# Kernel tuning notes

Hardware: AMD Instinct MI355X
Metric: run time of the kernel (lower is better)

The kernel has to match this reference:

```python
import jax, jax.numpy as jnp
import numpy as np
from jax import lax

DIM = 96; DSTATE = 16; DCONV = 3; EXPAND = 2
DINNER = DIM * EXPAND            # 192
DTRANK = (DIM + 15) // 16        # 6 = ceil(dim/16)
B = 4; H = 48; W = 48
BN_EPS = 1e-3
LN_EPS = 1e-5


def setup_inputs() -> dict:
    key = jax.random.key(0)
    ks = iter(jax.random.split(key, 32))
    def n(shape, s):
        return jax.random.normal(next(ks), shape, dtype=jnp.float32) * s
    inp = {}
    inp["feature"] = jax.random.normal(next(ks), (B, DIM, H, W), dtype=jnp.float32)
    inp["prediction"] = jax.random.normal(next(ks), (B, 1, H, W), dtype=jnp.float32)
    # norm_pred: BatchNorm2d(1) (eval mode, running stats)
    inp["bnp_g"] = jnp.ones((1,), jnp.float32)
    inp["bnp_b"] = jnp.zeros((1,), jnp.float32)
    inp["bnp_m"] = n((1,), 0.1)
    inp["bnp_v"] = jnp.ones((1,), jnp.float32) + jax.random.uniform(next(ks), (1,)) * 0.1
    # pre_proj: Conv1x1(no bias) + BN + GELU
    inp["pre_w"] = n((DIM, DIM), 0.05)
    inp["pre_bn_g"] = jnp.ones((DIM,), jnp.float32)
    inp["pre_bn_b"] = jnp.zeros((DIM,), jnp.float32)
    inp["pre_bn_m"] = n((DIM,), 0.1)
    inp["pre_bn_v"] = jnp.ones((DIM,), jnp.float32) + jax.random.uniform(next(ks), (DIM,)) * 0.1
    # norm_feature: LayerNorm(dim)
    inp["ln_g"] = jnp.ones((DIM,), jnp.float32)
    inp["ln_b"] = jnp.zeros((DIM,), jnp.float32)
    # SS2D params (VMamba)
    inp["in_proj_w"] = n((2 * DINNER, DIM), 0.05)
    inp["conv_w"] = n((DINNER, 1, DCONV, DCONV), 0.1)   # depthwise
    inp["conv_b"] = jnp.zeros((DINNER,), jnp.float32)
    inp["x_proj_w"] = n((4, DTRANK + 2 * DSTATE, DINNER), 0.05)
    inp["dt_w"] = n((4, DINNER, DTRANK), 0.1)
    inp["dt_b"] = n((4, DINNER), 0.1)
    # S4D-real init: A = -exp(A_logs), A_logs = log(1..N)
    inp["A_logs"] = jnp.log(jnp.tile(jnp.arange(1, DSTATE + 1, dtype=jnp.float32), (4 * DINNER, 1)))
    inp["Ds"] = jnp.ones((4 * DINNER,), jnp.float32)
    inp["onorm_g"] = jnp.ones((DINNER,), jnp.float32)
    inp["onorm_b"] = jnp.zeros((DINNER,), jnp.float32)
    inp["out_proj_w"] = n((DIM, DINNER), 0.05)
    # post_proj: Conv1x1(no bias) + BN + GELU
    inp["post_w"] = n((DIM, DIM), 0.05)
    inp["post_bn_g"] = jnp.ones((DIM,), jnp.float32)
    inp["post_bn_b"] = jnp.zeros((DIM,), jnp.float32)
    inp["post_bn_m"] = n((DIM,), 0.1)
    inp["post_bn_v"] = jnp.ones((DIM,), jnp.float32) + jax.random.uniform(next(ks), (DIM,)) * 0.1
    inp["gate"] = jnp.ones((1,), jnp.float32) * 0.5
    return inp


def _bn(x, g, b, m, v):
    # x: [B,C,H,W]; per-channel eval-mode batchnorm, eps=1e-3
    scale = g / jnp.sqrt(v + BN_EPS)
    return (x - m[None, :, None, None]) * scale[None, :, None, None] + b[None, :, None, None]


def _ln(x, g, b):
    mu = jnp.mean(x, axis=-1, keepdims=True)
    var = jnp.var(x, axis=-1, keepdims=True)
    return (x - mu) / jnp.sqrt(var + LN_EPS) * g + b


def _selective_scan(xs, dts, As, Bs, Cs, Ds, dt_bias):
    # xs,dts: [B,4,D,L]; As: [4,D,N]; Bs,Cs: [B,4,N,L]; Ds,dt_bias: [4,D]
    delta = jax.nn.softplus(dts + dt_bias[None, :, :, None])   # [B,4,D,L]
    u_t = jnp.moveaxis(xs, -1, 0)      # [L,B,4,D]
    d_t = jnp.moveaxis(delta, -1, 0)   # [L,B,4,D]
    B_t = jnp.moveaxis(Bs, -1, 0)      # [L,B,4,N]
    C_t = jnp.moveaxis(Cs, -1, 0)      # [L,B,4,N]
    h0 = jnp.zeros(xs.shape[:3] + (As.shape[-1],), xs.dtype)   # [B,4,D,N]
    def step(h, inp):
        u, d, Bm, Cm = inp
        dA = jnp.exp(d[..., None] * As[None])                     # [B,4,D,N]
        h = h * dA + (d * u)[..., None] * Bm[:, :, None, :]
        y = jnp.einsum('bkdn,bkn->bkd', h, Cm)
        return h, y
    _, ys = lax.scan(step, h0, (u_t, d_t, B_t, C_t))
    y = jnp.moveaxis(ys, 0, -1)        # [B,4,D,L]
    return y + Ds[None, :, :, None] * xs


def _ss2d(x_cl, in_proj_w, conv_w, conv_b, x_proj_w, dt_w, dt_b, A_logs, Ds,
          onorm_g, onorm_b, out_proj_w):
    Bsz, Hh, Ww, _ = x_cl.shape
    di = conv_w.shape[0]
    L = Hh * Ww
    xz = jnp.einsum('bhwc,oc->bhwo', x_cl, in_proj_w)
    x, z = jnp.split(xz, 2, axis=-1)
    xc = jnp.transpose(x, (0, 3, 1, 2))                           # [B,di,H,W]
    pad = (DCONV - 1) // 2
    xc = lax.conv_general_dilated(xc, conv_w, (1, 1), [(pad, pad), (pad, pad)],
                                  dimension_numbers=('NCHW', 'OIHW', 'NCHW'),
                                  feature_group_count=di) + conv_b[None, :, None, None]
    xc = jax.nn.silu(xc)
    # cross-scan: row-major, col-major, and their reverses
    x0 = xc.reshape(Bsz, di, L)
    x1 = jnp.transpose(xc, (0, 1, 3, 2)).reshape(Bsz, di, L)
    xhw = jnp.stack([x0, x1], axis=1)                             # [B,2,di,L]
    xs = jnp.concatenate([xhw, jnp.flip(xhw, axis=-1)], axis=1)   # [B,4,di,L]
    x_dbl = jnp.einsum('bkdl,kcd->bkcl', xs, x_proj_w)
    dts = x_dbl[:, :, :DTRANK]
    Bs = x_dbl[:, :, DTRANK:DTRANK + DSTATE]
    Cs = x_dbl[:, :, DTRANK + DSTATE:]
    dts = jnp.einsum('bkrl,kdr->bkdl', dts, dt_w)
    As = -jnp.exp(A_logs).reshape(4, di, DSTATE)
    out_y = _selective_scan(xs, dts, As, Bs, Cs, Ds.reshape(4, di), dt_b)  # [B,4,di,L]
    inv_y = jnp.flip(out_y[:, 2:4], axis=-1)
    wh = jnp.transpose(out_y[:, 1].reshape(Bsz, di, Ww, Hh), (0, 1, 3, 2)).reshape(Bsz, di, L)
    invwh = jnp.transpose(inv_y[:, 1].reshape(Bsz, di, Ww, Hh), (0, 1, 3, 2)).reshape(Bsz, di, L)
    y = out_y[:, 0] + inv_y[:, 0] + wh + invwh                    # [B,di,L]
    y = jnp.transpose(y.reshape(Bsz, di, Hh, Ww), (0, 2, 3, 1))   # [B,H,W,di]
    y = _ln(y, onorm_g, onorm_b)
    y = y * jax.nn.silu(z)
    return jnp.einsum('bhwd,od->bhwo', y, out_proj_w)


def reference(feature, prediction, bnp_g, bnp_b, bnp_m, bnp_v,
              pre_w, pre_bn_g, pre_bn_b, pre_bn_m, pre_bn_v, ln_g, ln_b,
              in_proj_w, conv_w, conv_b, x_proj_w, dt_w, dt_b, A_logs, Ds,
              onorm_g, onorm_b, out_proj_w,
              post_w, post_bn_g, post_bn_b, post_bn_m, post_bn_v, gate):
    pred_norm = _bn(prediction, bnp_g, bnp_b, bnp_m, bnp_v)
    reverse_mask = 1.0 - jax.nn.sigmoid(pred_norm)
    fm = feature * reverse_mask
    fp = jax.nn.gelu(_bn(jnp.einsum('bchw,oc->bohw', fm, pre_w),
                         pre_bn_g, pre_bn_b, pre_bn_m, pre_bn_v), approximate=False)
    x_cl = _ln(jnp.transpose(fp, (0, 2, 3, 1)), ln_g, ln_b)
    y = _ss2d(x_cl, in_proj_w, conv_w, conv_b, x_proj_w, dt_w, dt_b, A_logs, Ds,
              onorm_g, onorm_b, out_proj_w)
    yr = jnp.transpose(y, (0, 3, 1, 2))
    yr = jax.nn.gelu(_bn(jnp.einsum('bchw,oc->bohw', yr, post_w),
                         post_bn_g, post_bn_b, post_bn_m, post_bn_v), approximate=False)
    return feature + gate[0] * yr
```

## Files before the change

kernel.cpp:

```cpp
#include <hip/hip_runtime.h>
#include <math.h>

#define RFL(x) __builtin_amdgcn_readfirstlane(x)

constexpr int CDIM = 96;
constexpr int DI   = 192;
constexpr int HW   = 48;
constexpr int LL   = 2304;
constexpr int NK   = 4;
constexpr int DST  = 16;
constexpr int DTRK = 6;
constexpr int NCH  = 48;
constexpr int CHK  = 48;
constexpr float LOG2E  = 1.44269504088896f;
constexpr float CBN_EPS = 1e-3f;
constexpr float CLN_EPS = 1e-5f;

__device__ __forceinline__ int Tmap(int x){ return (x % HW) * HW + x / HW; }
__device__ __forceinline__ float siluf(float x){ return x / (1.f + __expf(-x)); }
__device__ __forceinline__ float geluf(float x){ return 0.5f * x * (1.f + erff(x * 0.70710678118654752f)); }
__device__ __forceinline__ int permp(int k, int l){
  if (k == 0) return l;
  if (k == 1) return Tmap(l);
  if (k == 2) return LL - 1 - l;
  return Tmap(LL - 1 - l);
}
__device__ __forceinline__ int lmap(int k, int p){
  if (k == 0) return p;
  if (k == 1) return Tmap(p);
  if (k == 2) return LL - 1 - p;
  return LL - 1 - Tmap(p);
}

__global__ __launch_bounds__(256) void mrr_k0_wcomb(
    const float* __restrict__ post_w, const float* __restrict__ opw, float* __restrict__ Wc)
{
  int idx = blockIdx.x * 256 + threadIdx.x;
  int o = idx / DI, d = idx % DI;
  float acc = 0.f;
  for (int c = 0; c < CDIM; ++c)
    acc = fmaf(post_w[o * CDIM + c], opw[c * DI + d], acc);
  Wc[idx] = acc;
}

__global__ __launch_bounds__(256) void mrr_k1_pre(
    const float* __restrict__ feature, const float* __restrict__ pred,
    const float* __restrict__ bnp_g, const float* __restrict__ bnp_b,
    const float* __restrict__ bnp_m, const float* __restrict__ bnp_v,
    const float* __restrict__ pre_w,
    const float* __restrict__ pbg, const float* __restrict__ pbb,
    const float* __restrict__ pbm, const float* __restrict__ pbv,
    const float* __restrict__ lng, const float* __restrict__ lnb,
    float* __restrict__ x_cl)
{
  __shared__ float s_fm[CDIM][64];
  __shared__ float s_red[8][64];
  __shared__ float s_mu[64], s_rs[64];
  int tid = threadIdx.x;
  int b = blockIdx.x / 36, p0 = (blockIdx.x % 36) * 64;

  if (tid < 64) {
    float pr = pred[b * LL + p0 + tid];
    float sc = bnp_g[0] * rsqrtf(bnp_v[0] + CBN_EPS);
    float pn = (pr - bnp_m[0]) * sc + bnp_b[0];
    s_mu[tid] = 1.f - 1.f / (1.f + __expf(-pn));
  }
  __syncthreads();
  #pragma unroll
  for (int e = 0; e < 24; ++e) {
    int f = e * 256 + tid;
    int c = f >> 6, px = f & 63;
    s_fm[c][px] = feature[(size_t)(b * CDIM + c) * LL + p0 + px] * s_mu[px];
  }
  __syncthreads();
  int lane = tid & 63;
  int wave = tid >> 6;
  int oc0 = RFL(wave * 24);
  float acc[24];
  #pragma unroll
  for (int j = 0; j < 24; ++j) acc[j] = 0.f;
  for (int c = 0; c < CDIM; c += 4) {
    float f0 = s_fm[c][lane], f1 = s_fm[c+1][lane];
    float f2 = s_fm[c+2][lane], f3 = s_fm[c+3][lane];
    #pragma unroll
    for (int j = 0; j < 24; ++j) {
      float4 w = *(const float4*)&pre_w[(oc0 + j) * CDIM + c];
      acc[j] = fmaf(w.x, f0, fmaf(w.y, f1, fmaf(w.z, f2, fmaf(w.w, f3, acc[j]))));
    }
  }
  float s = 0.f, s2 = 0.f;
  #pragma unroll
  for (int j = 0; j < 24; ++j) {
    int oc = oc0 + j;
    float sc = pbg[oc] * rsqrtf(pbv[oc] + CBN_EPS);
    float v = (acc[j] - pbm[oc]) * sc + pbb[oc];
    v = geluf(v);
    acc[j] = v; s += v; s2 = fmaf(v, v, s2);
  }
  s_red[wave][lane] = s; s_red[4 + wave][lane] = s2;
  __syncthreads();
  if (tid < 64) {
    float t1 = s_red[0][tid] + s_red[1][tid] + s_red[2][tid] + s_red[3][tid];
    float t2 = s_red[4][tid] + s_red[5][tid] + s_red[6][tid] + s_red[7][tid];
    float mu = t1 * (1.f / 96.f);
    float var = t2 * (1.f / 96.f) - mu * mu;
    s_mu[tid] = mu; s_rs[tid] = rsqrtf(var + CLN_EPS);
  }
  __syncthreads();
  float mu = s_mu[lane], rs = s_rs[lane];
  #pragma unroll
  for (int j = 0; j < 24; ++j) {
    int oc = oc0 + j;
    acc[j] = (acc[j] - mu) * rs * lng[oc] + lnb[oc];
  }
  float* dst = &x_cl[(size_t)(b * LL + p0 + lane) * CDIM + oc0];
  #pragma unroll
  for (int j = 0; j < 24; j += 4)
    *(float4*)(dst + j) = make_float4(acc[j], acc[j+1], acc[j+2], acc[j+3]);
}

__global__ __launch_bounds__(1024) void mrr_k2_inproj(
    const float* __restrict__ x_cl, const float* __restrict__ ipw,
    float* __restrict__ xb, float* __restrict__ szb)
{
  __shared__ float s_x[CDIM][65];
  int tid = threadIdx.x;
  int b = blockIdx.x / 36, p0 = (blockIdx.x % 36) * 64;
  #pragma unroll
  for (int e = 0; e < 6; ++e) {
    int f = e * 1024 + tid;
    int c = f % CDIM, px = f / CDIM;
    s_x[c][px] = x_cl[(size_t)(b * LL + p0 + px) * CDIM + c];
  }
  __syncthreads();
  int lane = tid & 63;
  int oc0 = RFL((tid >> 6) * 24);
  float acc[24];
  #pragma unroll
  for (int j = 0; j < 24; ++j) acc[j] = 0.f;
  for (int c = 0; c < CDIM; c += 4) {
    float f0 = s_x[c][lane], f1 = s_x[c+1][lane];
    float f2 = s_x[c+2][lane], f3 = s_x[c+3][lane];
    #pragma unroll
    for (int j = 0; j < 24; ++j) {
      float4 w = *(const float4*)&ipw[(oc0 + j) * CDIM + c];
      acc[j] = fmaf(w.x, f0, fmaf(w.y, f1, fmaf(w.z, f2, fmaf(w.w, f3, acc[j]))));
    }
  }
  int p = p0 + lane;
  if (oc0 < DI) {
    float* dst = &xb[(size_t)(b * LL + p) * DI + oc0];
    #pragma unroll
    for (int j = 0; j < 24; j += 4)
      *(float4*)(dst + j) = make_float4(acc[j], acc[j+1], acc[j+2], acc[j+3]);
  } else {
    #pragma unroll
    for (int j = 0; j < 24; ++j) acc[j] = siluf(acc[j]);
    float* dst = &szb[(size_t)(b * LL + p) * DI + (oc0 - DI)];
    #pragma unroll
    for (int j = 0; j < 24; j += 4)
      *(float4*)(dst + j) = make_float4(acc[j], acc[j+1], acc[j+2], acc[j+3]);
  }
}

__global__ __launch_bounds__(256) void mrr_k3_conv(
    const float* __restrict__ xb, const float* __restrict__ cw,
    const float* __restrict__ cb, float* __restrict__ xc)
{
  int idx = blockIdx.x * 256 + threadIdx.x;
  int d = idx % DI;
  int p = (idx / DI) % LL;
  int b = idx / (DI * LL);
  int h = p / HW, w = p % HW;
  float acc = cb[d];
  #pragma unroll
  for (int i = 0; i < 3; ++i) {
    int hh = h + i - 1;
    if (hh < 0 || hh >= HW) continue;
    #pragma unroll
    for (int j = 0; j < 3; ++j) {
      int ww = w + j - 1;
      if (ww < 0 || ww >= HW) continue;
      acc = fmaf(cw[d * 9 + i * 3 + j], xb[(size_t)(b * LL + hh * HW + ww) * DI + d], acc);
    }
  }
  xc[idx] = siluf(acc);
}

__global__ __launch_bounds__(640) void mrr_k4_proj(
    const float* __restrict__ xc, const float* __restrict__ xpw,
    const float* __restrict__ dtw, const float* __restrict__ dtb,
    float* __restrict__ delta, float* __restrict__ Bsb, float* __restrict__ Csb)
{
  __shared__ float s_u[DI][72];
  __shared__ float s_w[48][164];
  __shared__ float s_dtr[NK][DTRK][64];
  __shared__ float s_dtwf[NK * DI * DTRK];
  __shared__ float s_dtbf[NK * DI];
  int tid = threadIdx.x;
  int b = blockIdx.x / 36, p0 = (blockIdx.x % 36) * 64;
  int b4 = b * NK;

  for (int f = tid; f < DI * 64; f += 640) {
    int d_ = f % DI, px = f / DI;
    s_u[d_][px] = xc[(size_t)(b * LL + p0 + px) * DI + d_];
  }
  for (int f = tid; f < NK * DI * DTRK; f += 640) s_dtwf[f] = dtw[f];
  for (int f = tid; f < NK * DI; f += 640) s_dtbf[f] = dtb[f];

  int rg = tid >> 4;
  int pg = tid & 15;
  float acc[4][4];
  #pragma unroll
  for (int i = 0; i < 4; ++i)
    #pragma unroll
    for (int j = 0; j < 4; ++j) acc[i][j] = 0.f;

  for (int ch = 0; ch < 4; ++ch) {
    int c0 = ch * 48;
    if (ch) __syncthreads();
    for (int f = tid; f < 152 * 48; f += 640) {
      int cl = f % 48, row = f / 48;
      int kk = row / 38, rr = row % 38;
      s_w[cl][kk * 40 + rr] = xpw[row * DI + c0 + cl];
    }
    __syncthreads();
    #pragma unroll 4
    for (int cc = 0; cc < 48; ++cc) {
      float4 wv = *(const float4*)&s_w[cc][rg << 2];
      float4 uv = *(const float4*)&s_u[c0 + cc][pg << 2];
      acc[0][0] = fmaf(wv.x, uv.x, acc[0][0]); acc[0][1] = fmaf(wv.x, uv.y, acc[0][1]);
      acc[0][2] = fmaf(wv.x, uv.z, acc[0][2]); acc[0][3] = fmaf(wv.x, uv.w, acc[0][3]);
      acc[1][0] = fmaf(wv.y, uv.x, acc[1][0]); acc[1][1] = fmaf(wv.y, uv.y, acc[1][1]);
      acc[1][2] = fmaf(wv.y, uv.z, acc[1][2]); acc[1][3] = fmaf(wv.y, uv.w, acc[1][3]);
      acc[2][0] = fmaf(wv.z, uv.x, acc[2][0]); acc[2][1] = fmaf(wv.z, uv.y, acc[2][1]);
      acc[2][2] = fmaf(wv.z, uv.z, acc[2][2]); acc[2][3] = fmaf(wv.z, uv.w, acc[2][3]);
      acc[3][0] = fmaf(wv.w, uv.x, acc[3][0]); acc[3][1] = fmaf(wv.w, uv.y, acc[3][1]);
      acc[3][2] = fmaf(wv.w, uv.z, acc[3][2]); acc[3][3] = fmaf(wv.w, uv.w, acc[3][3]);
    }
  }

  #pragma unroll
  for (int i = 0; i < 4; ++i) {
    int rp = (rg << 2) + i;
    int kk = rp / 40, rr = rp % 40;
    if (rr < DTRK) {
      #pragma unroll
      for (int j = 0; j < 4; ++j) s_dtr[kk][rr][(pg << 2) + j] = acc[i][j];
    } else if (rr < DTRK + DST) {
      int n = rr - DTRK;
      #pragma unroll
      for (int j = 0; j < 4; ++j) {
        int l = lmap(kk, p0 + (pg << 2) + j);
        Bsb[(size_t)((b4 + kk) * LL + l) * DST + n] = acc[i][j];
      }
    } else if (rr < DTRK + 2 * DST) {
      int n = rr - DTRK - DST;
      #pragma unroll
      for (int j = 0; j < 4; ++j) {
        int l = lmap(kk, p0 + (pg << 2) + j);
        Csb[(size_t)((b4 + kk) * LL + l) * DST + n] = acc[i][j];
      }
    }
  }
  __syncthreads();

  int lane = tid & 63;
  int wv_ = tid >> 6;
  for (int unit = wv_; unit < 64; unit += 10) {
    int kk = unit >> 4, pxq = unit & 15;
    float dtr[6][4];
    #pragma unroll
    for (int rr = 0; rr < 6; ++rr)
      #pragma unroll
      for (int j = 0; j < 4; ++j)
        dtr[rr][j] = s_dtr[kk][rr][(pxq << 2) + j];
    #pragma unroll
    for (int dch = 0; dch < 3; ++dch) {
      int d_ = dch * 64 + lane;
      int kdl = kk * DI + d_;
      float w0 = s_dtwf[kdl * 6 + 0], w1 = s_dtwf[kdl * 6 + 1], w2 = s_dtwf[kdl * 6 + 2];
      float w3 = s_dtwf[kdl * 6 + 3], w4 = s_dtwf[kdl * 6 + 4], w5 = s_dtwf[kdl * 6 + 5];
      float bias = s_dtbf[kdl];
      #pragma unroll
      for (int j = 0; j < 4; ++j) {
        float sv = bias;
        sv = fmaf(w0, dtr[0][j], sv); sv = fmaf(w1, dtr[1][j], sv);
        sv = fmaf(w2, dtr[2][j], sv); sv = fmaf(w3, dtr[3][j], sv);
        sv = fmaf(w4, dtr[4][j], sv); sv = fmaf(w5, dtr[5][j], sv);
        float sp = fmaxf(sv, 0.f) + __logf(1.f + __expf(-fabsf(sv)));
        int l = lmap(kk, p0 + (pxq << 2) + j);
        delta[(size_t)((b4 + kk) * LL + l) * DI + d_] = sp;
      }
    }
  }
}

#define SSTEP(n, Bc, Cc) { float dA = exp2f(A2[n] * dv); hh[n] = fmaf(hh[n], dA, du * (Bc)); y = fmaf(hh[n], (Cc), y); }

__global__ __launch_bounds__(256) void mrr_k5_scan1(
    const float* __restrict__ delta, const float* __restrict__ xc,
    const float* __restrict__ Bsb, const float* __restrict__ Csb,
    const float* __restrict__ A_logs,
    float* __restrict__ yb, float* __restrict__ hend, float* __restrict__ Ssum)
{
  int lane = threadIdx.x & 63;
  int wid = RFL(blockIdx.x * 4 + (threadIdx.x >> 6));
  int c = wid % NCH;
  int r = wid / NCH;
  int dch = r % 3;
  int k = (r / 3) % NK;
  int b = r / (3 * NK);
  int d = dch * 64 + lane;
  int kd = k * DI + d;

  float A2[16];
  {
    const float4* Ap = (const float4*)&A_logs[(size_t)kd * 16];
    #pragma unroll
    for (int i = 0; i < 4; ++i) {
      float4 a = Ap[i];
      A2[4*i+0] = -exp2f(a.x * LOG2E) * LOG2E;
      A2[4*i+1] = -exp2f(a.y * LOG2E) * LOG2E;
      A2[4*i+2] = -exp2f(a.z * LOG2E) * LOG2E;
      A2[4*i+3] = -exp2f(a.w * LOG2E) * LOG2E;
    }
  }
  float hh[16];
  #pragma unroll
  for (int n = 0; n < 16; ++n) hh[n] = 0.f;
  float S = 0.f;
  int l0 = c * CHK;
  int bk = b * NK + k;
  size_t ebase = (size_t)(bk * LL + l0) * DI + d;
  size_t bbase = (size_t)(bk * LL + l0) * DST;
  float dv = delta[ebase];
  float u  = xc[(size_t)(b * LL + permp(k, l0)) * DI + d];
  const float4* Bp = (const float4*)(Bsb + bbase);
  const float4* Cp = (const float4*)(Csb + bbase);
  float4 B0 = Bp[0], B1 = Bp[1], B2 = Bp[2], B3 = Bp[3];
  float4 C0 = Cp[0], C1 = Cp[1], C2 = Cp[2], C3 = Cp[3];
  for (int t = 0; t < CHK; ++t) {
    int tn = (t < CHK - 1) ? t + 1 : t;
    float ndv = delta[ebase + (size_t)tn * DI];
    float nu  = xc[(size_t)(b * LL + permp(k, l0 + tn)) * DI + d];
    const float4* nBp = (const float4*)(Bsb + bbase + (size_t)tn * DST);
    const float4* nCp = (const float4*)(Csb + bbase + (size_t)tn * DST);
    float4 nB0 = nBp[0], nB1 = nBp[1], nB2 = nBp[2], nB3 = nBp[3];
    float4 nC0 = nCp[0], nC1 = nCp[1], nC2 = nCp[2], nC3 = nCp[3];
    float du = dv * u;
    float y = 0.f;
    SSTEP(0,  B0.x, C0.x) SSTEP(1,  B0.y, C0.y) SSTEP(2,  B0.z, C0.z) SSTEP(3,  B0.w, C0.w)
    SSTEP(4,  B1.x, C1.x) SSTEP(5,  B1.y, C1.y) SSTEP(6,  B1.z, C1.z) SSTEP(7,  B1.w, C1.w)
    SSTEP(8,  B2.x, C2.x) SSTEP(9,  B2.y, C2.y) SSTEP(10, B2.z, C2.z) SSTEP(11, B2.w, C2.w)
    SSTEP(12, B3.x, C3.x) SSTEP(13, B3.y, C3.y) SSTEP(14, B3.z, C3.z) SSTEP(15, B3.w, C3.w)
    yb[ebase + (size_t)t * DI] = y;
    S += dv;
    dv = ndv; u = nu;
    B0 = nB0; B1 = nB1; B2 = nB2; B3 = nB3;
    C0 = nC0; C1 = nC1; C2 = nC2; C3 = nC3;
  }
  int gg = bk * 3 + dch;
  size_t hb = ((size_t)(gg * NCH + c) * 64 + lane) * 16;
  float4* Hp = (float4*)&hend[hb];
  Hp[0] = make_float4(hh[0], hh[1], hh[2], hh[3]);
  Hp[1] = make_float4(hh[4], hh[5], hh[6], hh[7]);
  Hp[2] = make_float4(hh[8], hh[9], hh[10], hh[11]);
  Hp[3] = make_float4(hh[12], hh[13], hh[14], hh[15]);
  Ssum[(size_t)(gg * NCH + c) * 64 + lane] = S;
}

__global__ __launch_bounds__(1024) void mrr_k5_mid(
    const float* __restrict__ hend, const float* __restrict__ Ssum,
    const float* __restrict__ A_logs, float* __restrict__ hinit)
{
  int t = blockIdx.x * 1024 + threadIdx.x;
  int n = t & 15;
  int g = t >> 4;
  int ln = g & 63;
  int gg = g >> 6;
  int dch = gg % 3;
  int k = (gg / 3) % NK;
  int d = dch * 64 + ln;
  float AL = A_logs[(size_t)(k * DI + d) * 16 + n];
  float A2 = -exp2f(AL * LOG2E) * LOG2E;
  float hi = 0.f;
  for (int c = 0; c < NCH; ++c) {
    size_t a = ((size_t)(gg * NCH + c) * 64 + ln) * 16 + n;
    hinit[a] = hi;
    float S = Ssum[(size_t)(gg * NCH + c) * 64 + ln];
    hi = hend[a] + exp2f(A2 * S) * hi;
  }
}

#define CSTEP(n, Cc) { float e = exp2f(A2[n] * cum); corr = fmaf(e * gi[n], (Cc), corr); }

__global__ __launch_bounds__(256) void mrr_k5_scan2(
    const float* __restrict__ delta, const float* __restrict__ Csb,
    const float* __restrict__ A_logs, const float* __restrict__ hinit,
    float* __restrict__ yb)
{
  int lane = threadIdx.x & 63;
  int wid = RFL(blockIdx.x * 4 + (threadIdx.x >> 6));
  int c = wid % NCH;
  if (c == 0) return;
  int r = wid / NCH;
  int dch = r % 3;
  int k = (r / 3) % NK;
  int b = r / (3 * NK);
  int d = dch * 64 + lane;
  int kd = k * DI + d;
  float A2[16];
  {
    const float4* Ap = (const float4*)&A_logs[(size_t)kd * 16];
    #pragma unroll
    for (int i = 0; i < 4; ++i) {
      float4 a = Ap[i];
      A2[4*i+0] = -exp2f(a.x * LOG2E) * LOG2E;
      A2[4*i+1] = -exp2f(a.y * LOG2E) * LOG2E;
      A2[4*i+2] = -exp2f(a.z * LOG2E) * LOG2E;
      A2[4*i+3] = -exp2f(a.w * LOG2E) * LOG2E;
    }
  }
  int bk = b * NK + k;
  int gg = bk * 3 + dch;
  float gi[16];
  {
    const float4* Gp = (const float4*)&hinit[((size_t)(gg * NCH + c) * 64 + lane) * 16];
    float4 g0 = Gp[0], g1 = Gp[1], g2 = Gp[2], g3 = Gp[3];
    gi[0]=g0.x; gi[1]=g0.y; gi[2]=g0.z; gi[3]=g0.w;
    gi[4]=g1.x; gi[5]=g1.y; gi[6]=g1.z; gi[7]=g1.w;
    gi[8]=g2.x; gi[9]=g2.y; gi[10]=g2.z; gi[11]=g2.w;
    gi[12]=g3.x; gi[13]=g3.y; gi[14]=g3.z; gi[15]=g3.w;
  }
  int l0 = c * CHK;
  size_t ebase = (size_t)(bk * LL + l0) * DI + d;
  size_t bbase = (size_t)(bk * LL + l0) * DST;
  float cum = 0.f;
  float dv = delta[ebase];
  const float4* Cp = (const float4*)(Csb + bbase);
  float4 C0 = Cp[0], C1 = Cp[1], C2 = Cp[2], C3 = Cp[3];
  for (int t = 0; t < CHK; ++t) {
    int tn = (t < CHK - 1) ? t + 1 : t;
    float ndv = delta[ebase + (size_t)tn * DI];
    const float4* nCp = (const float4*)(Csb + bbase + (size_t)tn * DST);
    float4 nC0 = nCp[0], nC1 = nCp[1], nC2 = nCp[2], nC3 = nCp[3];
    cum += dv;
    float corr = 0.f;
    CSTEP(0,  C0.x) CSTEP(1,  C0.y) CSTEP(2,  C0.z) CSTEP(3,  C0.w)
    CSTEP(4,  C1.x) CSTEP(5,  C1.y) CSTEP(6,  C1.z) CSTEP(7,  C1.w)
    CSTEP(8,  C2.x) CSTEP(9,  C2.y) CSTEP(10, C2.z) CSTEP(11, C2.w)
    CSTEP(12, C3.x) CSTEP(13, C3.y) CSTEP(14, C3.z) CSTEP(15, C3.w)
    yb[ebase + (size_t)t * DI] += corr;
    dv = ndv;
    C0 = nC0; C1 = nC1; C2 = nC2; C3 = nC3;
  }
}

__global__ __launch_bounds__(1024) void mrr_k6_out(
    const float* __restrict__ yb, const float* __restrict__ xc,
    const float* __restrict__ szb, const float* __restrict__ Ds,
    const float* __restrict__ ong, const float* __restrict__ onb,
    const float* __restrict__ Wc,
    const float* __restrict__ qbg, const float* __restrict__ qbb,
    const float* __restrict__ qbm, const float* __restrict__ qbv,
    const float* __restrict__ feature, const float* __restrict__ gate,
    float* __restrict__ out)
{
  __shared__ float s_t[DI][65];
  __shared__ float s_red[32][64];
  __shared__ float s_mu[64], s_rs[64];
  int tid = threadIdx.x;
  int b = blockIdx.x / 36, p0 = (blockIdx.x % 36) * 64;
  int b4 = b * NK;
  #pragma unroll
  for (int e = 0; e < 12; ++e) {
    int f = e * 1024 + tid;
    int d = f % DI, px = f / DI;
    int p = p0 + px;
    int tp = Tmap(p);
    float t0 = yb[(size_t)((b4 + 0) * LL + p) * DI + d];
    float t1 = yb[(size_t)((b4 + 1) * LL + tp) * DI + d];
    float t2 = yb[(size_t)((b4 + 2) * LL + (LL - 1 - p)) * DI + d];
    float t3 = yb[(size_t)((b4 + 3) * LL + (LL - 1 - tp)) * DI + d];
    float Dv = Ds[d] + Ds[DI + d] + Ds[2 * DI + d] + Ds[3 * DI + d];
    float tv = t0 + t1 + t2 + t3 + Dv * xc[(size_t)(b * LL + p) * DI + d];
    s_t[d][px] = tv;
  }
  __syncthreads();
  {
    int q = tid >> 6, px = tid & 63;
    float s = 0.f, s2 = 0.f;
    #pragma unroll
    for (int i = 0; i < 12; ++i) {
      float v = s_t[q * 12 + i][px];
      s += v; s2 = fmaf(v, v, s2);
    }
    s_red[q][px] = s; s_red[16 + q][px] = s2;
  }
  __syncthreads();
  if (tid < 64) {
    float s = 0.f, s2 = 0.f;
    #pragma unroll
    for (int q = 0; q < 16; ++q) { s += s_red[q][tid]; s2 += s_red[16 + q][tid]; }
    float mu = s * (1.f / (float)DI);
    float var = s2 * (1.f / (float)DI) - mu * mu;
    s_mu[tid] = mu; s_rs[tid] = rsqrtf(var + CLN_EPS);
  }
  __syncthreads();
  #pragma unroll
  for (int e = 0; e < 12; ++e) {
    int f = e * 1024 + tid;
    int d = f % DI, px = f / DI;
    int p = p0 + px;
    float v = s_t[d][px];
    v = (v - s_mu[px]) * s_rs[px] * ong[d] + onb[d];
    v *= szb[(size_t)(b * LL + p) * DI + d];
    s_t[d][px] = v;
  }
  __syncthreads();
  int lane = tid & 63;
  int o0 = RFL((tid >> 6) * 6);
  float acc[6] = {0.f, 0.f, 0.f, 0.f, 0.f, 0.f};
  for (int dd = 0; dd < DI; dd += 4) {
    float f0 = s_t[dd][lane], f1 = s_t[dd+1][lane];
    float f2 = s_t[dd+2][lane], f3 = s_t[dd+3][lane];
    #pragma unroll
    for (int j = 0; j < 6; ++j) {
      float4 w = *(const float4*)&Wc[(o0 + j) * DI + dd];
      acc[j] = fmaf(w.x, f0, fmaf(w.y, f1, fmaf(w.z, f2, fmaf(w.w, f3, acc[j]))));
    }
  }
  float gt = gate[0];
  #pragma unroll
  for (int j = 0; j < 6; ++j) {
    int o = o0 + j;
    float sc = qbg[o] * rsqrtf(qbv[o] + CBN_EPS);
    float v = (acc[j] - qbm[o]) * sc + qbb[o];
    v = geluf(v);
    size_t oi = (size_t)(b * CDIM + o) * LL + p0 + lane;
    out[oi] = feature[oi] + gt * v;
  }
}

extern "C" void kernel_launch(void* const* d_in, const int* in_sizes, int n_in,
                              void* d_out, int out_size, void* d_ws, size_t ws_size,
                              hipStream_t stream)
{
  (void)in_sizes; (void)n_in; (void)out_size; (void)ws_size;
  const float* feature    = (const float*)d_in[0];
  const float* prediction = (const float*)d_in[1];
  const float* bnp_g      = (const float*)d_in[2];
  const float* bnp_b      = (const float*)d_in[3];
  const float* bnp_m      = (const float*)d_in[4];
  const float* bnp_v      = (const float*)d_in[5];
  const float* pre_w      = (const float*)d_in[6];
  const float* pre_bn_g   = (const float*)d_in[7];
  const float* pre_bn_b   = (const float*)d_in[8];
  const float* pre_bn_m   = (const float*)d_in[9];
  const float* pre_bn_v   = (const float*)d_in[10];
  const float* ln_g       = (const float*)d_in[11];
  const float* ln_b       = (const float*)d_in[12];
  const float* in_proj_w  = (const float*)d_in[13];
  const float* conv_w     = (const float*)d_in[14];
  const float* conv_b     = (const float*)d_in[15];
  const float* x_proj_w   = (const float*)d_in[16];
  const float* dt_w       = (const float*)d_in[17];
  const float* dt_b       = (const float*)d_in[18];
  const float* A_logs     = (const float*)d_in[19];
  const float* Ds         = (const float*)d_in[20];
  const float* onorm_g    = (const float*)d_in[21];
  const float* onorm_b    = (const float*)d_in[22];
  const float* out_proj_w = (const float*)d_in[23];
  const float* post_w     = (const float*)d_in[24];
  const float* post_bn_g  = (const float*)d_in[25];
  const float* post_bn_b  = (const float*)d_in[26];
  const float* post_bn_m  = (const float*)d_in[27];
  const float* post_bn_v  = (const float*)d_in[28];
  const float* gate       = (const float*)d_in[29];
  float* out = (float*)d_out;

  float* ws    = (float*)d_ws;
  float* Wc    = ws;
  float* x_cl  = Wc    + 18432;
  float* xb    = x_cl  + 884736;
  float* szb   = xb    + 1769472;
  float* xcb   = szb   + 1769472;
  float* dlt   = xcb   + 1769472;
  float* Bsb   = dlt   + 7077888;
  float* Csb   = Bsb   + 589824;
  float* yb    = Csb   + 589824;
  float* hend  = yb    + 7077888;
  float* hinit = hend  + 2359296;
  float* Ss    = hinit + 2359296;

  mrr_k0_wcomb<<<dim3(72), dim3(256), 0, stream>>>(post_w, out_proj_w, Wc);
  mrr_k1_pre<<<dim3(144), dim3(256), 0, stream>>>(feature, prediction,
      bnp_g, bnp_b, bnp_m, bnp_v, pre_w,
      pre_bn_g, pre_bn_b, pre_bn_m, pre_bn_v, ln_g, ln_b, x_cl);
  mrr_k2_inproj<<<dim3(144), dim3(1024), 0, stream>>>(x_cl, in_proj_w, xb, szb);
  mrr_k3_conv<<<dim3(6912), dim3(256), 0, stream>>>(xb, conv_w, conv_b, xcb);
  mrr_k4_proj<<<dim3(144), dim3(640), 0, stream>>>(xcb, x_proj_w, dt_w, dt_b, dlt, Bsb, Csb);
  mrr_k5_scan1<<<dim3(576), dim3(256), 0, stream>>>(dlt, xcb, Bsb, Csb, A_logs, yb, hend, Ss);
  mrr_k5_mid<<<dim3(48), dim3(1024), 0, stream>>>(hend, Ss, A_logs, hinit);
  mrr_k5_scan2<<<dim3(576), dim3(256), 0, stream>>>(dlt, Csb, A_logs, hinit, yb);
  mrr_k6_out<<<dim3(144), dim3(1024), 0, stream>>>(yb, xcb, szb, Ds, onorm_g, onorm_b,
      Wc, post_bn_g, post_bn_b, post_bn_m, post_bn_v, feature, gate, out);
}
```

Measured before the change: 388.5 us.

## Split kernels into more blocks, vectorise conv, store cumulative delta for scan2

Several kernels are repartitioned into smaller blocks (pre, inproj, out) so the GPU runs more workgroups. The depthwise conv now handles four channels per thread with float4 loads, using a transposed weight buffer. The scan uses twice as many chunks of half the length and splits the y accumulation across four independent registers. scan1 writes the running delta sum over delta in place, so scan2 reads it directly instead of re-accumulating. The middle pass converts hend to hinit in place, and together with the larger chunk count this changes the workspace layout and adds more inter-chunk serial work.

```diff
diff --git a/kernel.cpp b/kernel.cpp
--- a/kernel.cpp
+++ b/kernel.cpp
@@ -10,8 +10,8 @@
 constexpr int NK   = 4;
 constexpr int DST  = 16;
 constexpr int DTRK = 6;
-constexpr int NCH  = 48;
-constexpr int CHK  = 48;
+constexpr int NCH  = 96;
+constexpr int CHK  = 24;
 constexpr float LOG2E  = 1.44269504088896f;
 constexpr float CBN_EPS = 1e-3f;
 constexpr float CLN_EPS = 1e-5f;
@@ -33,14 +33,21 @@
 }
 
 __global__ __launch_bounds__(256) void mrr_k0_wcomb(
-    const float* __restrict__ post_w, const float* __restrict__ opw, float* __restrict__ Wc)
+    const float* __restrict__ post_w, const float* __restrict__ opw,
+    const float* __restrict__ conv_w, float* __restrict__ Wc, float* __restrict__ cwT)
 {
   int idx = blockIdx.x * 256 + threadIdx.x;
-  int o = idx / DI, d = idx % DI;
-  float acc = 0.f;
-  for (int c = 0; c < CDIM; ++c)
-    acc = fmaf(post_w[o * CDIM + c], opw[c * DI + d], acc);
-  Wc[idx] = acc;
+  if (idx < CDIM * DI) {
+    int o = idx / DI, d = idx % DI;
+    float acc = 0.f;
+    for (int c = 0; c < CDIM; ++c)
+      acc = fmaf(post_w[o * CDIM + c], opw[c * DI + d], acc);
+    Wc[idx] = acc;
+  } else if (idx < CDIM * DI + 9 * DI) {
+    int t = idx - CDIM * DI;
+    int tap = t / DI, d = t % DI;
+    cwT[tap * DI + d] = conv_w[d * 9 + tap];
+  }
 }
 
 __global__ __launch_bounds__(256) void mrr_k1_pre(
@@ -53,88 +60,95 @@
     const float* __restrict__ lng, const float* __restrict__ lnb,
     float* __restrict__ x_cl)
 {
-  __shared__ float s_fm[CDIM][64];
-  __shared__ float s_red[8][64];
-  __shared__ float s_mu[64], s_rs[64];
+  __shared__ float s_fm[CDIM][33];
+  __shared__ float s_red[16][32];
+  __shared__ float s_mu[32], s_rs[32], s_msk[32];
   int tid = threadIdx.x;
-  int b = blockIdx.x / 36, p0 = (blockIdx.x % 36) * 64;
-
-  if (tid < 64) {
+  int b = blockIdx.x / 72, p0 = (blockIdx.x % 72) * 32;
+
+  if (tid < 32) {
     float pr = pred[b * LL + p0 + tid];
     float sc = bnp_g[0] * rsqrtf(bnp_v[0] + CBN_EPS);
     float pn = (pr - bnp_m[0]) * sc + bnp_b[0];
-    s_mu[tid] = 1.f - 1.f / (1.f + __expf(-pn));
-  }
-  __syncthreads();
-  #pragma unroll
-  for (int e = 0; e < 24; ++e) {
+    s_msk[tid] = 1.f - 1.f / (1.f + __expf(-pn));
+  }
+  __syncthreads();
+  #pragma unroll
+  for (int e = 0; e < 12; ++e) {
     int f = e * 256 + tid;
-    int c = f >> 6, px = f & 63;
-    s_fm[c][px] = feature[(size_t)(b * CDIM + c) * LL + p0 + px] * s_mu[px];
+    int c = f >> 5, px = f & 31;
+    s_fm[c][px] = feature[(size_t)(b * CDIM + c) * LL + p0 + px] * s_msk[px];
   }
   __syncthreads();
   int lane = tid & 63;
   int wave = tid >> 6;
-  int oc0 = RFL(wave * 24);
-  float acc[24];
-  #pragma unroll
-  for (int j = 0; j < 24; ++j) acc[j] = 0.f;
+  int px = lane & 31, oh = lane >> 5;
+  int o0 = wave * 24 + oh * 12;
+  float acc[12];
+  #pragma unroll
+  for (int j = 0; j < 12; ++j) acc[j] = 0.f;
   for (int c = 0; c < CDIM; c += 4) {
-    float f0 = s_fm[c][lane], f1 = s_fm[c+1][lane];
-    float f2 = s_fm[c+2][lane], f3 = s_fm[c+3][lane];
-    #pragma unroll
-    for (int j = 0; j < 24; ++j) {
-      float4 w = *(const float4*)&pre_w[(oc0 + j) * CDIM + c];
+    float f0 = s_fm[c][px], f1 = s_fm[c+1][px];
+    float f2 = s_fm[c+2][px], f3 = s_fm[c+3][px];
+    #pragma unroll
+    for (int j = 0; j < 12; ++j) {
+      float4 w = *(const float4*)&pre_w[(o0 + j) * CDIM + c];
       acc[j] = fmaf(w.x, f0, fmaf(w.y, f1, fmaf(w.z, f2, fmaf(w.w, f3, acc[j]))));
     }
   }
   float s = 0.f, s2 = 0.f;
   #pragma unroll
-  for (int j = 0; j < 24; ++j) {
-    int oc = oc0 + j;
+  for (int j = 0; j < 12; ++j) {
+    int oc = o0 + j;
     float sc = pbg[oc] * rsqrtf(pbv[oc] + CBN_EPS);
     float v = (acc[j] - pbm[oc]) * sc + pbb[oc];
     v = geluf(v);
     acc[j] = v; s += v; s2 = fmaf(v, v, s2);
   }
-  s_red[wave][lane] = s; s_red[4 + wave][lane] = s2;
-  __syncthreads();
-  if (tid < 64) {
-    float t1 = s_red[0][tid] + s_red[1][tid] + s_red[2][tid] + s_red[3][tid];
-    float t2 = s_red[4][tid] + s_red[5][tid] + s_red[6][tid] + s_red[7][tid];
+  int grp = wave * 2 + oh;
+  s_red[grp][px] = s; s_red[8 + grp][px] = s2;
+  __syncthreads();
+  if (tid < 32) {
+    float t1 = 0.f, t2 = 0.f;
+    #pragma unroll
+    for (int q = 0; q < 8; ++q) { t1 += s_red[q][tid]; t2 += s_red[8 + q][tid]; }
     float mu = t1 * (1.f / 96.f);
     float var = t2 * (1.f / 96.f) - mu * mu;
     s_mu[tid] = mu; s_rs[tid] = rsqrtf(var + CLN_EPS);
   }
   __syncthreads();
-  float mu = s_mu[lane], rs = s_rs[lane];
-  #pragma unroll
-  for (int j = 0; j < 24; ++j) {
-    int oc = oc0 + j;
+  float mu = s_mu[px], rs = s_rs[px];
+  #pragma unroll
+  for (int j = 0; j < 12; ++j) {
+    int oc = o0 + j;
     acc[j] = (acc[j] - mu) * rs * lng[oc] + lnb[oc];
   }
-  float* dst = &x_cl[(size_t)(b * LL + p0 + lane) * CDIM + oc0];
-  #pragma unroll
-  for (int j = 0; j < 24; j += 4)
+  float* dst = &x_cl[(size_t)(b * LL + p0 + px) * CDIM + o0];
+  #pragma unroll
+  for (int j = 0; j < 12; j += 4)
     *(float4*)(dst + j) = make_float4(acc[j], acc[j+1], acc[j+2], acc[j+3]);
 }
 
-__global__ __launch_bounds__(1024) void mrr_k2_inproj(
+__global__ __launch_bounds__(256) void mrr_k2_inproj(
     const float* __restrict__ x_cl, const float* __restrict__ ipw,
     float* __restrict__ xb, float* __restrict__ szb)
 {
   __shared__ float s_x[CDIM][65];
   int tid = threadIdx.x;
-  int b = blockIdx.x / 36, p0 = (blockIdx.x % 36) * 64;
-  #pragma unroll
-  for (int e = 0; e < 6; ++e) {
-    int f = e * 1024 + tid;
+  int blk = blockIdx.x;
+  int b = blk / 144;
+  int rem = blk % 144;
+  int p0 = (rem % 36) * 64;
+  int q = rem / 36;
+  #pragma unroll
+  for (int e = 0; e < 24; ++e) {
+    int f = e * 256 + tid;
     int c = f % CDIM, px = f / CDIM;
     s_x[c][px] = x_cl[(size_t)(b * LL + p0 + px) * CDIM + c];
   }
   __syncthreads();
   int lane = tid & 63;
-  int oc0 = RFL((tid >> 6) * 24);
+  int oc0 = RFL(q * 96 + (tid >> 6) * 24);
   float acc[24];
   #pragma unroll
   for (int j = 0; j < 24; ++j) acc[j] = 0.f;
@@ -164,15 +178,15 @@
 }
 
 __global__ __launch_bounds__(256) void mrr_k3_conv(
-    const float* __restrict__ xb, const float* __restrict__ cw,
+    const float* __restrict__ xb, const float* __restrict__ cwT,
     const float* __restrict__ cb, float* __restrict__ xc)
 {
   int idx = blockIdx.x * 256 + threadIdx.x;
-  int d = idx % DI;
-  int p = (idx / DI) % LL;
-  int b = idx / (DI * LL);
+  int dg = idx % 48;
+  int p = (idx / 48) % LL;
+  int b = idx / (48 * LL);
   int h = p / HW, w = p % HW;
-  float acc = cb[d];
+  float4 acc = ((const float4*)cb)[dg];
   #pragma unroll
   for (int i = 0; i < 3; ++i) {
     int hh = h + i - 1;
@@ -181,10 +195,16 @@
     for (int j = 0; j < 3; ++j) {
       int ww = w + j - 1;
       if (ww < 0 || ww >= HW) continue;
-      acc = fmaf(cw[d * 9 + i * 3 + j], xb[(size_t)(b * LL + hh * HW + ww) * DI + d], acc);
-    }
-  }
-  xc[idx] = siluf(acc);
+      float4 wv = ((const float4*)&cwT[(i * 3 + j) * DI])[dg];
+      float4 xv = *(const float4*)&xb[(size_t)(b * LL + hh * HW + ww) * DI + dg * 4];
+      acc.x = fmaf(wv.x, xv.x, acc.x);
+      acc.y = fmaf(wv.y, xv.y, acc.y);
+      acc.z = fmaf(wv.z, xv.z, acc.z);
+      acc.w = fmaf(wv.w, xv.w, acc.w);
+    }
+  }
+  acc.x = siluf(acc.x); acc.y = siluf(acc.y); acc.z = siluf(acc.z); acc.w = siluf(acc.w);
+  *(float4*)&xc[(size_t)(b * LL + p) * DI + dg * 4] = acc;
 }
 
 __global__ __launch_bounds__(640) void mrr_k4_proj(
@@ -296,12 +316,13 @@
   }
 }
 
-#define SSTEP(n, Bc, Cc) { float dA = exp2f(A2[n] * dv); hh[n] = fmaf(hh[n], dA, du * (Bc)); y = fmaf(hh[n], (Cc), y); }
+#define SSTEP(n, Bc, Cc, yy) { float dA = exp2f(A2[n] * dv); hh[n] = fmaf(hh[n], dA, du * (Bc)); yy = fmaf(hh[n], (Cc), yy); }
 
 __global__ __launch_bounds__(256) void mrr_k5_scan1(
-    const float* __restrict__ delta, const float* __restrict__ xc,
+    const float* __restrict__ xc,
     const float* __restrict__ Bsb, const float* __restrict__ Csb,
     const float* __restrict__ A_logs,
+    float* __restrict__ delta,
     float* __restrict__ yb, float* __restrict__ hend, float* __restrict__ Ssum)
 {
   int lane = threadIdx.x & 63;
@@ -349,13 +370,14 @@
     float4 nB0 = nBp[0], nB1 = nBp[1], nB2 = nBp[2], nB3 = nBp[3];
     float4 nC0 = nCp[0], nC1 = nCp[1], nC2 = nCp[2], nC3 = nCp[3];
     float du = dv * u;
-    float y = 0.f;
-    SSTEP(0,  B0.x, C0.x) SSTEP(1,  B0.y, C0.y) SSTEP(2,  B0.z, C0.z) SSTEP(3,  B0.w, C0.w)
-    SSTEP(4,  B1.x, C1.x) SSTEP(5,  B1.y, C1.y) SSTEP(6,  B1.z, C1.z) SSTEP(7,  B1.w, C1.w)
-    SSTEP(8,  B2.x, C2.x) SSTEP(9,  B2.y, C2.y) SSTEP(10, B2.z, C2.z) SSTEP(11, B2.w, C2.w)
-    SSTEP(12, B3.x, C3.x) SSTEP(13, B3.y, C3.y) SSTEP(14, B3.z, C3.z) SSTEP(15, B3.w, C3.w)
-    yb[ebase + (size_t)t * DI] = y;
+    float y0 = 0.f, y1 = 0.f, y2 = 0.f, y3 = 0.f;
+    SSTEP(0,  B0.x, C0.x, y0) SSTEP(1,  B0.y, C0.y, y1) SSTEP(2,  B0.z, C0.z, y2) SSTEP(3,  B0.w, C0.w, y3)
+    SSTEP(4,  B1.x, C1.x, y0) SSTEP(5,  B1.y, C1.y, y1) SSTEP(6,  B1.z, C1.z, y2) SSTEP(7,  B1.w, C1.w, y3)
+    SSTEP(8,  B2.x, C2.x, y0) SSTEP(9,  B2.y, C2.y, y1) SSTEP(10, B2.z, C2.z, y2) SSTEP(11, B2.w, C2.w, y3)
+    SSTEP(12, B3.x, C3.x, y0) SSTEP(13, B3.y, C3.y, y1) SSTEP(14, B3.z, C3.z, y2) SSTEP(15, B3.w, C3.w, y3)
+    yb[ebase + (size_t)t * DI] = (y0 + y1) + (y2 + y3);
     S += dv;
+    delta[ebase + (size_t)t * DI] = S;
     dv = ndv; u = nu;
     B0 = nB0; B1 = nB1; B2 = nB2; B3 = nB3;
     C0 = nC0; C1 = nC1; C2 = nC2; C3 = nC3;
@@ -371,8 +393,8 @@
 }
 
 __global__ __launch_bounds__(1024) void mrr_k5_mid(
-    const float* __restrict__ hend, const float* __restrict__ Ssum,
-    const float* __restrict__ A_logs, float* __restrict__ hinit)
+    float* __restrict__ hend, const float* __restrict__ Ssum,
+    const float* __restrict__ A_logs)
 {
   int t = blockIdx.x * 1024 + threadIdx.x;
   int n = t & 15;
@@ -387,16 +409,17 @@
   float hi = 0.f;
   for (int c = 0; c < NCH; ++c) {
     size_t a = ((size_t)(gg * NCH + c) * 64 + ln) * 16 + n;
-    hinit[a] = hi;
+    float tmp = hend[a];
     float S = Ssum[(size_t)(gg * NCH + c) * 64 + ln];
-    hi = hend[a] + exp2f(A2 * S) * hi;
-  }
-}
-
-#define CSTEP(n, Cc) { float e = exp2f(A2[n] * cum); corr = fmaf(e * gi[n], (Cc), corr); }
+    hend[a] = hi;
+    hi = tmp + exp2f(A2 * S) * hi;
+  }
+}
+
+#define CSTEP(n, Cc, yy) { float e = exp2f(A2[n] * cum); yy = fmaf(e * gi[n], (Cc), yy); }
 
 __global__ __launch_bounds__(256) void mrr_k5_scan2(
-    const float* __restrict__ delta, const float* __restrict__ Csb,
+    const float* __restrict__ cumd, const float* __restrict__ Csb,
     const float* __restrict__ A_logs, const float* __restrict__ hinit,
     float* __restrict__ yb)
 {
@@ -436,28 +459,21 @@
   int l0 = c * CHK;
   size_t ebase = (size_t)(bk * LL + l0) * DI + d;
   size_t bbase = (size_t)(bk * LL + l0) * DST;
-  float cum = 0.f;
-  float dv = delta[ebase];
-  const float4* Cp = (const float4*)(Csb + bbase);
-  float4 C0 = Cp[0], C1 = Cp[1], C2 = Cp[2], C3 = Cp[3];
+  #pragma unroll 2
   for (int t = 0; t < CHK; ++t) {
-    int tn = (t < CHK - 1) ? t + 1 : t;
-    float ndv = delta[ebase + (size_t)tn * DI];
-    const float4* nCp = (const float4*)(Csb + bbase + (size_t)tn * DST);
-    float4 nC0 = nCp[0], nC1 = nCp[1], nC2 = nCp[2], nC3 = nCp[3];
-    cum += dv;
-    float corr = 0.f;
-    CSTEP(0,  C0.x) CSTEP(1,  C0.y) CSTEP(2,  C0.z) CSTEP(3,  C0.w)
-    CSTEP(4,  C1.x) CSTEP(5,  C1.y) CSTEP(6,  C1.z) CSTEP(7,  C1.w)
-    CSTEP(8,  C2.x) CSTEP(9,  C2.y) CSTEP(10, C2.z) CSTEP(11, C2.w)
-    CSTEP(12, C3.x) CSTEP(13, C3.y) CSTEP(14, C3.z) CSTEP(15, C3.w)
-    yb[ebase + (size_t)t * DI] += corr;
-    dv = ndv;
-    C0 = nC0; C1 = nC1; C2 = nC2; C3 = nC3;
-  }
-}
-
-__global__ __launch_bounds__(1024) void mrr_k6_out(
+    float cum = cumd[ebase + (size_t)t * DI];
+    const float4* Cp = (const float4*)(Csb + bbase + (size_t)t * DST);
+    float4 C0 = Cp[0], C1 = Cp[1], C2 = Cp[2], C3 = Cp[3];
+    float y0 = 0.f, y1 = 0.f, y2 = 0.f, y3 = 0.f;
+    CSTEP(0,  C0.x, y0) CSTEP(1,  C0.y, y1) CSTEP(2,  C0.z, y2) CSTEP(3,  C0.w, y3)
+    CSTEP(4,  C1.x, y0) CSTEP(5,  C1.y, y1) CSTEP(6,  C1.z, y2) CSTEP(7,  C1.w, y3)
+    CSTEP(8,  C2.x, y0) CSTEP(9,  C2.y, y1) CSTEP(10, C2.z, y2) CSTEP(11, C2.w, y3)
+    CSTEP(12, C3.x, y0) CSTEP(13, C3.y, y1) CSTEP(14, C3.z, y2) CSTEP(15, C3.w, y3)
+    yb[ebase + (size_t)t * DI] += (y0 + y1) + (y2 + y3);
+  }
+}
+
+__global__ __launch_bounds__(512) void mrr_k6_out(
     const float* __restrict__ yb, const float* __restrict__ xc,
     const float* __restrict__ szb, const float* __restrict__ Ds,
     const float* __restrict__ ong, const float* __restrict__ onb,
@@ -467,15 +483,15 @@
     const float* __restrict__ feature, const float* __restrict__ gate,
     float* __restrict__ out)
 {
-  __shared__ float s_t[DI][65];
-  __shared__ float s_red[32][64];
-  __shared__ float s_mu[64], s_rs[64];
+  __shared__ float s_t[DI][33];
+  __shared__ float s_red[32][32];
+  __shared__ float s_mu[32], s_rs[32];
   int tid = threadIdx.x;
-  int b = blockIdx.x / 36, p0 = (blockIdx.x % 36) * 64;
+  int b = blockIdx.x / 72, p0 = (blockIdx.x % 72) * 32;
   int b4 = b * NK;
   #pragma unroll
   for (int e = 0; e < 12; ++e) {
-    int f = e * 1024 + tid;
+    int f = e * 512 + tid;
     int d = f % DI, px = f / DI;
     int p = p0 + px;
     int tp = Tmap(p);
@@ -489,7 +505,7 @@
   }
   __syncthreads();
   {
-    int q = tid >> 6, px = tid & 63;
+    int q = tid >> 5, px = tid & 31;
     float s = 0.f, s2 = 0.f;
     #pragma unroll
     for (int i = 0; i < 12; ++i) {
@@ -499,7 +515,7 @@
     s_red[q][px] = s; s_red[16 + q][px] = s2;
   }
   __syncthreads();
-  if (tid < 64) {
+  if (tid < 32) {
     float s = 0.f, s2 = 0.f;
     #pragma unroll
     for (int q = 0; q < 16; ++q) { s += s_red[q][tid]; s2 += s_red[16 + q][tid]; }
@@ -510,7 +526,7 @@
   __syncthreads();
   #pragma unroll
   for (int e = 0; e < 12; ++e) {
-    int f = e * 1024 + tid;
+    int f = e * 512 + tid;
     int d = f % DI, px = f / DI;
     int p = p0 + px;
     float v = s_t[d][px];
@@ -520,11 +536,13 @@
   }
   __syncthreads();
   int lane = tid & 63;
-  int o0 = RFL((tid >> 6) * 6);
+  int wave = tid >> 6;
+  int px = lane & 31, oh = lane >> 5;
+  int o0 = wave * 12 + oh * 6;
   float acc[6] = {0.f, 0.f, 0.f, 0.f, 0.f, 0.f};
   for (int dd = 0; dd < DI; dd += 4) {
-    float f0 = s_t[dd][lane], f1 = s_t[dd+1][lane];
-    float f2 = s_t[dd+2][lane], f3 = s_t[dd+3][lane];
+    float f0 = s_t[dd][px], f1 = s_t[dd+1][px];
+    float f2 = s_t[dd+2][px], f3 = s_t[dd+3][px];
     #pragma unroll
     for (int j = 0; j < 6; ++j) {
       float4 w = *(const float4*)&Wc[(o0 + j) * DI + dd];
@@ -538,7 +556,7 @@
     float sc = qbg[o] * rsqrtf(qbv[o] + CBN_EPS);
     float v = (acc[j] - qbm[o]) * sc + qbb[o];
     v = geluf(v);
-    size_t oi = (size_t)(b * CDIM + o) * LL + p0 + lane;
+    size_t oi = (size_t)(b * CDIM + o) * LL + p0 + px;
     out[oi] = feature[oi] + gt * v;
   }
 }
@@ -591,19 +609,19 @@
   float* Csb   = Bsb   + 589824;
   float* yb    = Csb   + 589824;
   float* hend  = yb    + 7077888;
-  float* hinit = hend  + 2359296;
-  float* Ss    = hinit + 2359296;
-
-  mrr_k0_wcomb<<<dim3(72), dim3(256), 0, stream>>>(post_w, out_proj_w, Wc);
-  mrr_k1_pre<<<dim3(144), dim3(256), 0, stream>>>(feature, prediction,
+  float* Ss    = hend  + 4718592;
+  float* cwT   = Ss    + 294912;
+
+  mrr_k0_wcomb<<<dim3(79), dim3(256), 0, stream>>>(post_w, out_proj_w, conv_w, Wc, cwT);
+  mrr_k1_pre<<<dim3(288), dim3(256), 0, stream>>>(feature, prediction,
       bnp_g, bnp_b, bnp_m, bnp_v, pre_w,
       pre_bn_g, pre_bn_b, pre_bn_m, pre_bn_v, ln_g, ln_b, x_cl);
-  mrr_k2_inproj<<<dim3(144), dim3(1024), 0, stream>>>(x_cl, in_proj_w, xb, szb);
-  mrr_k3_conv<<<dim3(6912), dim3(256), 0, stream>>>(xb, conv_w, conv_b, xcb);
+  mrr_k2_inproj<<<dim3(576), dim3(256), 0, stream>>>(x_cl, in_proj_w, xb, szb);
+  mrr_k3_conv<<<dim3(1728), dim3(256), 0, stream>>>(xb, cwT, conv_b, xcb);
   mrr_k4_proj<<<dim3(144), dim3(640), 0, stream>>>(xcb, x_proj_w, dt_w, dt_b, dlt, Bsb, Csb);
-  mrr_k5_scan1<<<dim3(576), dim3(256), 0, stream>>>(dlt, xcb, Bsb, Csb, A_logs, yb, hend, Ss);
-  mrr_k5_mid<<<dim3(48), dim3(1024), 0, stream>>>(hend, Ss, A_logs, hinit);
-  mrr_k5_scan2<<<dim3(576), dim3(256), 0, stream>>>(dlt, Csb, A_logs, hinit, yb);
-  mrr_k6_out<<<dim3(144), dim3(1024), 0, stream>>>(yb, xcb, szb, Ds, onorm_g, onorm_b,
+  mrr_k5_scan1<<<dim3(1152), dim3(256), 0, stream>>>(xcb, Bsb, Csb, A_logs, dlt, yb, hend, Ss);
+  mrr_k5_mid<<<dim3(48), dim3(1024), 0, stream>>>(hend, Ss, A_logs);
+  mrr_k5_scan2<<<dim3(1152), dim3(256), 0, stream>>>(dlt, Csb, A_logs, hend, yb);
+  mrr_k6_out<<<dim3(288), dim3(512), 0, stream>>>(yb, xcb, szb, Ds, onorm_g, onorm_b,
       Wc, post_bn_g, post_bn_b, post_bn_m, post_bn_v, feature, gate, out);
 }
```

New measurement: 383.7 us. About the same (-1.2%).
